# Performance work log

Measured on AMD Instinct MI355X. Metric: run time of the kernel, lower is better.

Reference implementation:

```python
import jax, jax.numpy as jnp
import numpy as np
import math

B_, H_, W_ = 2, 32, 32
DM, DS = 192, 16
RK = math.ceil(DM / 16)  # dt_rank 'auto'
DI = 2 * DM              # d_inner = expand_factor * d_model


def setup_inputs() -> dict:
    key = jax.random.key(0)
    ks = jax.random.split(key, 8)
    x = jax.random.normal(ks[0], (B_, H_, W_, DM), jnp.float32)
    W_in = jax.random.normal(ks[1], (DM, DI), jnp.float32) * 0.02
    b_in = jnp.zeros((DI,), jnp.float32)
    W_x = jax.random.normal(ks[2], (DI, 2 * RK + 2 * DS), jnp.float32) * 0.02
    b_x = jnp.zeros((2 * RK + 2 * DS,), jnp.float32)
    std = RK ** -0.5
    W_dtT = jax.random.uniform(ks[3], (RK, DI), jnp.float32, -std, std)
    W_dtL = jax.random.uniform(ks[4], (RK, DI), jnp.float32, -std, std)
    # dt bias init exactly as in the torch module
    dt = jnp.exp(jax.random.uniform(ks[5], (DI,), jnp.float32)
                 * (math.log(0.1) - math.log(0.001)) + math.log(0.001))
    dt = jnp.clip(dt, 1e-4)
    inv_dt = dt + jnp.log(-jnp.expm1(-dt))
    A = jnp.tile(jnp.arange(1, DS + 1, dtype=jnp.float32), (DI, 1))
    AT_log = jnp.log(A)
    AL_log = jnp.log(A)
    D = jnp.ones((DI,), jnp.float32)
    W_out = jax.random.normal(ks[6], (DI, DM), jnp.float32) * 0.02
    b_out = jnp.zeros((DM,), jnp.float32)
    return dict(x=x, W_in=W_in, b_in=b_in, W_x=W_x, b_x=b_x,
                W_dtT=W_dtT, b_dtT=inv_dt, W_dtL=W_dtL, b_dtL=inv_dt,
                AT_log=AT_log, AL_log=AL_log, D=D, W_out=W_out, b_out=b_out)


def _wavefront_scan(dAT, dAL, bx):
    """2D wavefront linear recurrence over an (H, W) grid.
    h[i,j] = 0.5*dAT[i,j]*h[i-1,j] + 0.5*dAL[i,j]*h[i,j-1] + bx[i,j]
    Inputs: (B, H, W, d_inner, d_state). Sequential over rows (lax.scan),
    parallel linear recurrence along columns (associative_scan)."""
    def combine(c1, c2):
        a1, u1 = c1
        a2, u2 = c2
        return a2 * a1, a2 * u1 + u2

    def row_step(h_prev, row):
        dAT_r, dAL_r, bx_r = row                     # (B, W, di, ds)
        u = 0.5 * dAT_r * h_prev + bx_r              # top contribution folded in
        a = 0.5 * dAL_r
        _, h = jax.lax.associative_scan(combine, (a, u), axis=1)
        return h, h

    rows = (jnp.moveaxis(dAT, 1, 0), jnp.moveaxis(dAL, 1, 0), jnp.moveaxis(bx, 1, 0))
    h0 = jnp.zeros(dAT.shape[:1] + dAT.shape[2:], dAT.dtype)
    _, hs = jax.lax.scan(row_step, h0, rows)         # (H, B, W, di, ds)
    return jnp.moveaxis(hs, 0, 1)                    # (B, H, W, di, ds)


def reference(x, W_in, b_in, W_x, b_x, W_dtT, b_dtT, W_dtL, b_dtL,
              AT_log, AL_log, D, W_out, b_out):
    # in_proj + GELU (torch nn.GELU default = exact erf)
    h = jax.nn.gelu(x @ W_in + b_in, approximate=False)   # (B,H,W,DI)
    # proj_and_discretise
    dbc = h @ W_x + b_x
    dT, dL, Bm, Cm = jnp.split(dbc, [RK, 2 * RK, 2 * RK + DS], axis=-1)
    deltaT = jax.nn.softplus(dT @ W_dtT + b_dtT)          # (B,H,W,DI)
    deltaL = jax.nn.softplus(dL @ W_dtL + b_dtL)
    AT = -jnp.exp(AT_log)                                  # (DI,DS)
    AL = -jnp.exp(AL_log)
    dAT = jnp.exp(deltaT[..., None] * AT)                  # (B,H,W,DI,DS)
    dAL = jnp.exp(deltaL[..., None] * AL)
    BXT = (deltaT * h)[..., None] * Bm[..., None, :]       # delta*B*x
    BXL = (deltaL * h)[..., None] * Bm[..., None, :]
    # 2D wavefront selective scan
    hs = _wavefront_scan(dAT, dAL, 0.5 * (BXT + BXL))
    y = jnp.einsum('bhwds,bhws->bhwd', hs, Cm) + h * D
    # act2 + out_proj
    y = jax.nn.gelu(y, approximate=False)
    return y @ W_out + b_out
```

## Files before the change

### kernel.cpp

```cpp
#include <hip/hip_runtime.h>
#include <math.h>

#define TOK 2048
#define DMOD 192
#define DI 384
#define DS 16
#define RK 12
#define NCOL 56
#define HH 32
#define WW 32
#define BB 2
#define TA 8
#define HSP 388

__device__ __forceinline__ float gelu_exact(float x) {
    return 0.5f * x * (1.0f + erff(x * 0.70710678118654752f));
}
__device__ __forceinline__ float softplus_f(float x) {
    return (x > 20.0f) ? x : log1pf(expf(x));
}
__device__ __forceinline__ float bperm(int byte_addr, float v) {
    return __uint_as_float((unsigned)__builtin_amdgcn_ds_bpermute(
        byte_addr, (int)__float_as_uint(v)));
}

__global__ void k0_transWx(const float* __restrict__ W_x, float* __restrict__ W_xT) {
    int c = blockIdx.x, k = threadIdx.x;
    W_xT[c * DI + k] = W_x[k * NCOL + c];
}

__global__ __launch_bounds__(DI) void K_A(
        const float* __restrict__ x, const float* __restrict__ W_in,
        const float* __restrict__ b_in, const float* __restrict__ W_xT,
        const float* __restrict__ b_x, const float* __restrict__ W_dtT,
        const float* __restrict__ b_dtT, const float* __restrict__ W_dtL,
        const float* __restrict__ b_dtL,
        float* __restrict__ ht, float* __restrict__ dTt, float* __restrict__ dLt,
        float* __restrict__ Bs, float* __restrict__ Cs) {
    __shared__ float xs[TA * DMOD];
    __shared__ float hs[TA * HSP];
    __shared__ float dbcS[TA][NCOL];
    int tid = threadIdx.x;
    int tok0 = blockIdx.x * TA;

    const float* xg = x + (long)tok0 * DMOD;
#pragma unroll
    for (int q = 0; q < 4; ++q) xs[q * DI + tid] = xg[q * DI + tid];
    __syncthreads();

    float acc[TA];
    float bi = b_in[tid];
#pragma unroll
    for (int t = 0; t < TA; ++t) acc[t] = bi;
    for (int k = 0; k < DMOD; k += 4) {
        float w0 = W_in[(k + 0) * DI + tid];
        float w1 = W_in[(k + 1) * DI + tid];
        float w2 = W_in[(k + 2) * DI + tid];
        float w3 = W_in[(k + 3) * DI + tid];
#pragma unroll
        for (int t = 0; t < TA; ++t) {
            float4 xv = *(const float4*)&xs[t * DMOD + k];
            acc[t] = fmaf(xv.x, w0, acc[t]);
            acc[t] = fmaf(xv.y, w1, acc[t]);
            acc[t] = fmaf(xv.z, w2, acc[t]);
            acc[t] = fmaf(xv.w, w3, acc[t]);
        }
    }
#pragma unroll
    for (int t = 0; t < TA; ++t) hs[t * HSP + tid] = gelu_exact(acc[t]);
    __syncthreads();

    for (int oi = tid; oi < TA * NCOL; oi += DI) {
        int tk = oi / NCOL, c = oi - tk * NCOL;
        float p = b_x[c];
        const float* hrow = &hs[tk * HSP];
        const float4* wr = (const float4*)(W_xT + c * DI);
        for (int k = 0; k < DI; k += 4) {
            float4 hv = *(const float4*)&hrow[k];
            float4 wv = wr[k >> 2];
            p = fmaf(hv.x, wv.x, p);  p = fmaf(hv.y, wv.y, p);
            p = fmaf(hv.z, wv.z, p);  p = fmaf(hv.w, wv.w, p);
        }
        dbcS[tk][c] = p;
    }
    __syncthreads();

    int d = tid;
    float aT[TA], aL[TA];
    float bT = b_dtT[d], bL = b_dtL[d];
#pragma unroll
    for (int t = 0; t < TA; ++t) { aT[t] = bT; aL[t] = bL; }
#pragma unroll
    for (int r = 0; r < RK; ++r) {
        float wT = W_dtT[r * DI + d];
        float wL = W_dtL[r * DI + d];
#pragma unroll
        for (int t = 0; t < TA; ++t) {
            aT[t] = fmaf(dbcS[t][r],      wT, aT[t]);
            aL[t] = fmaf(dbcS[t][RK + r], wL, aL[t]);
        }
    }
    int b = tok0 >> 10;
    long ob = (long)(b * DI + d) * 1024 + (tok0 & 1023);
    float v[TA];
#pragma unroll
    for (int t = 0; t < TA; ++t) v[t] = softplus_f(aT[t]);
    *(float4*)&dTt[ob]     = make_float4(v[0], v[1], v[2], v[3]);
    *(float4*)&dTt[ob + 4] = make_float4(v[4], v[5], v[6], v[7]);
#pragma unroll
    for (int t = 0; t < TA; ++t) v[t] = softplus_f(aL[t]);
    *(float4*)&dLt[ob]     = make_float4(v[0], v[1], v[2], v[3]);
    *(float4*)&dLt[ob + 4] = make_float4(v[4], v[5], v[6], v[7]);
#pragma unroll
    for (int t = 0; t < TA; ++t) v[t] = hs[t * HSP + d];
    *(float4*)&ht[ob]     = make_float4(v[0], v[1], v[2], v[3]);
    *(float4*)&ht[ob + 4] = make_float4(v[4], v[5], v[6], v[7]);
    if (tid < 128) {
        int s = tid >> 3, tt = tid & 7;
        long o = (long)(b * DS + s) * 1024 + (tok0 & 1023) + tt;
        Bs[o] = dbcS[tt][2 * RK + s];
        Cs[o] = dbcS[tt][2 * RK + DS + s];
    }
}

__global__ __launch_bounds__(256) void k3_scan(
        const float* __restrict__ dTt, const float* __restrict__ dLt,
        const float* __restrict__ ht, const float* __restrict__ Bs,
        const float* __restrict__ Cs, const float* __restrict__ AT_log,
        const float* __restrict__ AL_log, const float* __restrict__ Dv,
        float* __restrict__ yt) {
    __shared__ float part[8][HH][WW];
    int bd = blockIdx.x;
    int b = bd / DI, d = bd - b * DI;
    int tid = threadIdx.x;
    int w = tid >> 6, lane = tid & 63;
    int s1 = lane >> 5, j = lane & 31;
    int p = w * 2 + s1;

    float AT0 = -__expf(AT_log[d * DS + 2 * p]);
    float AT1 = -__expf(AT_log[d * DS + 2 * p + 1]);
    float AL0 = -__expf(AL_log[d * DS + 2 * p]);
    float AL1 = -__expf(AL_log[d * DS + 2 * p + 1]);

    const float* dTr = dTt + (long)bd * 1024;
    const float* dLr = dLt + (long)bd * 1024;
    const float* hr  = ht  + (long)bd * 1024;
    const float* B0r = Bs + (long)(b * DS + 2 * p) * 1024;
    const float* B1r = B0r + 1024;
    const float* C0r = Cs + (long)(b * DS + 2 * p) * 1024;
    const float* C1r = C0r + 1024;

    int ba1  = ((j >= 1  ? lane - 1  : lane) << 2);
    int ba2  = ((j >= 2  ? lane - 2  : lane) << 2);
    int ba4  = ((j >= 4  ? lane - 4  : lane) << 2);
    int ba8  = ((j >= 8  ? lane - 8  : lane) << 2);
    int ba16 = ((j >= 16 ? lane - 16 : lane) << 2);

    float hp0 = 0.f, hp1 = 0.f;
    float nT = dTr[j], nL = dLr[j], nh = hr[j];
    float nB0 = B0r[j], nB1 = B1r[j], nC0 = C0r[j], nC1 = C1r[j];

#pragma unroll 1
    for (int i = 0; i < HH; ++i) {
        float cT = nT, cL = nL, chv = nh;
        float cB0 = nB0, cB1 = nB1, cC0 = nC0, cC1 = nC1;
        int nx = (i + 1 < HH) ? (i + 1) * 32 + j : j;
        nT = dTr[nx]; nL = dLr[nx]; nh = hr[nx];
        nB0 = B0r[nx]; nB1 = B1r[nx]; nC0 = C0r[nx]; nC1 = C1r[nx];

        float g  = 0.5f * (cT + cL) * chv;
        float a0 = 0.5f * __expf(cL * AL0);
        float a1 = 0.5f * __expf(cL * AL1);
        float u0 = fmaf(0.5f * __expf(cT * AT0), hp0, g * cB0);
        float u1 = fmaf(0.5f * __expf(cT * AT1), hp1, g * cB1);

#define SCAN_STEP(BA, OFF)                                            \
        {                                                             \
            float au0 = bperm(BA, a0), uu0 = bperm(BA, u0);           \
            float au1 = bperm(BA, a1), uu1 = bperm(BA, u1);           \
            bool m = (j >= OFF);                                      \
            uu0 = m ? uu0 : 0.f;  au0 = m ? au0 : 1.f;                \
            uu1 = m ? uu1 : 0.f;  au1 = m ? au1 : 1.f;                \
            u0 = fmaf(a0, uu0, u0);  a0 *= au0;                       \
            u1 = fmaf(a1, uu1, u1);  a1 *= au1;                       \
        }
        SCAN_STEP(ba1, 1)  SCAN_STEP(ba2, 2)  SCAN_STEP(ba4, 4)
        SCAN_STEP(ba8, 8)  SCAN_STEP(ba16, 16)
#undef SCAN_STEP

        hp0 = u0;  hp1 = u1;
        part[p][i][j] = fmaf(u0, cC0, u1 * cC1);
    }
    __syncthreads();

    float Dd = Dv[d];
    float* yr = yt + (long)bd * 1024;
#pragma unroll
    for (int q = 0; q < 4; ++q) {
        int cell = q * 256 + tid;
        float sum = part[0][0][cell] + part[1][0][cell] + part[2][0][cell] +
                    part[3][0][cell] + part[4][0][cell] + part[5][0][cell] +
                    part[6][0][cell] + part[7][0][cell];
        yr[cell] = gelu_exact(sum + hr[cell] * Dd);
    }
}

__global__ __launch_bounds__(DMOD) void K_out(
        const float* __restrict__ yt, const float* __restrict__ W_out,
        const float* __restrict__ b_out, float* __restrict__ out) {
    int n = threadIdx.x;
    int tok0 = blockIdx.x * TA;
    int b = tok0 >> 10;
    const float* yb = yt + (long)b * DI * 1024 + (tok0 & 1023);
    float acc[TA];
    float bo = b_out[n];
#pragma unroll
    for (int t = 0; t < TA; ++t) acc[t] = bo;
    for (int dd = 0; dd < DI; ++dd) {
        float w = W_out[dd * DMOD + n];
        const float* yp = yb + (long)dd * 1024;
        float4 y0 = *(const float4*)yp;
        float4 y1 = *(const float4*)(yp + 4);
        acc[0] = fmaf(y0.x, w, acc[0]);  acc[1] = fmaf(y0.y, w, acc[1]);
        acc[2] = fmaf(y0.z, w, acc[2]);  acc[3] = fmaf(y0.w, w, acc[3]);
        acc[4] = fmaf(y1.x, w, acc[4]);  acc[5] = fmaf(y1.y, w, acc[5]);
        acc[6] = fmaf(y1.z, w, acc[6]);  acc[7] = fmaf(y1.w, w, acc[7]);
    }
#pragma unroll
    for (int t = 0; t < TA; ++t)
        out[(long)(tok0 + t) * DMOD + n] = acc[t];
}

extern "C" void kernel_launch(void* const* d_in, const int* in_sizes, int n_in,
                              void* d_out, int out_size, void* d_ws, size_t ws_size,
                              hipStream_t stream) {
    const float* x      = (const float*)d_in[0];
    const float* W_in   = (const float*)d_in[1];
    const float* b_in   = (const float*)d_in[2];
    const float* W_x    = (const float*)d_in[3];
    const float* b_x    = (const float*)d_in[4];
    const float* W_dtT  = (const float*)d_in[5];
    const float* b_dtT  = (const float*)d_in[6];
    const float* W_dtL  = (const float*)d_in[7];
    const float* b_dtL  = (const float*)d_in[8];
    const float* AT_log = (const float*)d_in[9];
    const float* AL_log = (const float*)d_in[10];
    const float* Dv     = (const float*)d_in[11];
    const float* W_out  = (const float*)d_in[12];
    const float* b_out  = (const float*)d_in[13];
    float* out = (float*)d_out;

    float* ws = (float*)d_ws;
    const long NE = (long)BB * DI * 1024;
    float* ht   = ws;
    float* dTt  = ws + NE;
    float* dLt  = ws + 2 * NE;
    float* Bs   = ws + 3 * NE;
    float* Cs   = Bs + (long)BB * DS * 1024;
    float* W_xT = Cs + (long)BB * DS * 1024;
    float* yt   = dTt;

    k0_transWx<<<NCOL, DI, 0, stream>>>(W_x, W_xT);
    K_A<<<TOK / TA, DI, 0, stream>>>(x, W_in, b_in, W_xT, b_x,
                                     W_dtT, b_dtT, W_dtL, b_dtL,
                                     ht, dTt, dLt, Bs, Cs);
    k3_scan<<<BB * DI, 256, 0, stream>>>(dTt, dLt, ht, Bs, Cs,
                                         AT_log, AL_log, Dv, yt);
    K_out<<<TOK / TA, DMOD, 0, stream>>>(yt, W_out, b_out, out);
}
```

Before: 177.8 us.

## Split projection kernel and compute delta softplus inside scan kernel

Replaces the monolithic K_A kernel with a separate in_proj+GELU kernel (more blocks, 128 threads) and a dedicated x_proj kernel that writes all 56 dbc columns channel-major. The dt projection and softplus move into the scan kernel, which computes deltaT/deltaL for its channel into shared memory, so the full-size dT/dL tensors no longer make a round trip through global memory. The W_x transpose kernel is dropped and the output projection tile shrinks to 4 tokens for more parallelism. In exchange, every scan block recomputes the 24-term dt projection from global dbc, and there are smaller tiles with less weight reuse.

```diff
diff --git a/kernel.cpp b/kernel.cpp
--- a/kernel.cpp
+++ b/kernel.cpp
@@ -10,8 +10,6 @@
 #define HH 32
 #define WW 32
 #define BB 2
-#define TA 8
-#define HSP 388
 
 __device__ __forceinline__ float gelu_exact(float x) {
     return 0.5f * x * (1.0f + erff(x * 0.70710678118654752f));
@@ -24,41 +22,30 @@
         byte_addr, (int)__float_as_uint(v)));
 }
 
-__global__ void k0_transWx(const float* __restrict__ W_x, float* __restrict__ W_xT) {
-    int c = blockIdx.x, k = threadIdx.x;
-    W_xT[c * DI + k] = W_x[k * NCOL + c];
-}
-
-__global__ __launch_bounds__(DI) void K_A(
+__global__ __launch_bounds__(128) void K_h(
         const float* __restrict__ x, const float* __restrict__ W_in,
-        const float* __restrict__ b_in, const float* __restrict__ W_xT,
-        const float* __restrict__ b_x, const float* __restrict__ W_dtT,
-        const float* __restrict__ b_dtT, const float* __restrict__ W_dtL,
-        const float* __restrict__ b_dtL,
-        float* __restrict__ ht, float* __restrict__ dTt, float* __restrict__ dLt,
-        float* __restrict__ Bs, float* __restrict__ Cs) {
-    __shared__ float xs[TA * DMOD];
-    __shared__ float hs[TA * HSP];
-    __shared__ float dbcS[TA][NCOL];
-    int tid = threadIdx.x;
-    int tok0 = blockIdx.x * TA;
-
+        const float* __restrict__ b_in, float* __restrict__ h_tm,
+        float* __restrict__ ht) {
+    __shared__ float xs[4 * DMOD];
+    int tx = threadIdx.x;
+    int n = blockIdx.x * 128 + tx;
+    int tok0 = blockIdx.y * 4;
     const float* xg = x + (long)tok0 * DMOD;
 #pragma unroll
-    for (int q = 0; q < 4; ++q) xs[q * DI + tid] = xg[q * DI + tid];
+    for (int q = 0; q < 6; ++q) xs[q * 128 + tx] = xg[q * 128 + tx];
     __syncthreads();
-
-    float acc[TA];
-    float bi = b_in[tid];
-#pragma unroll
-    for (int t = 0; t < TA; ++t) acc[t] = bi;
+    float acc[4];
+    float bi = b_in[n];
+#pragma unroll
+    for (int t = 0; t < 4; ++t) acc[t] = bi;
+#pragma unroll 2
     for (int k = 0; k < DMOD; k += 4) {
-        float w0 = W_in[(k + 0) * DI + tid];
-        float w1 = W_in[(k + 1) * DI + tid];
-        float w2 = W_in[(k + 2) * DI + tid];
-        float w3 = W_in[(k + 3) * DI + tid];
-#pragma unroll
-        for (int t = 0; t < TA; ++t) {
+        float w0 = W_in[(k + 0) * DI + n];
+        float w1 = W_in[(k + 1) * DI + n];
+        float w2 = W_in[(k + 2) * DI + n];
+        float w3 = W_in[(k + 3) * DI + n];
+#pragma unroll
+        for (int t = 0; t < 4; ++t) {
             float4 xv = *(const float4*)&xs[t * DMOD + k];
             acc[t] = fmaf(xv.x, w0, acc[t]);
             acc[t] = fmaf(xv.y, w1, acc[t]);
@@ -66,73 +53,83 @@
             acc[t] = fmaf(xv.w, w3, acc[t]);
         }
     }
-#pragma unroll
-    for (int t = 0; t < TA; ++t) hs[t * HSP + tid] = gelu_exact(acc[t]);
-    __syncthreads();
-
-    for (int oi = tid; oi < TA * NCOL; oi += DI) {
-        int tk = oi / NCOL, c = oi - tk * NCOL;
-        float p = b_x[c];
-        const float* hrow = &hs[tk * HSP];
-        const float4* wr = (const float4*)(W_xT + c * DI);
-        for (int k = 0; k < DI; k += 4) {
-            float4 hv = *(const float4*)&hrow[k];
-            float4 wv = wr[k >> 2];
-            p = fmaf(hv.x, wv.x, p);  p = fmaf(hv.y, wv.y, p);
-            p = fmaf(hv.z, wv.z, p);  p = fmaf(hv.w, wv.w, p);
-        }
-        dbcS[tk][c] = p;
-    }
-    __syncthreads();
-
-    int d = tid;
-    float aT[TA], aL[TA];
-    float bT = b_dtT[d], bL = b_dtL[d];
-#pragma unroll
-    for (int t = 0; t < TA; ++t) { aT[t] = bT; aL[t] = bL; }
-#pragma unroll
-    for (int r = 0; r < RK; ++r) {
-        float wT = W_dtT[r * DI + d];
-        float wL = W_dtL[r * DI + d];
-#pragma unroll
-        for (int t = 0; t < TA; ++t) {
-            aT[t] = fmaf(dbcS[t][r],      wT, aT[t]);
-            aL[t] = fmaf(dbcS[t][RK + r], wL, aL[t]);
-        }
-    }
-    int b = tok0 >> 10;
-    long ob = (long)(b * DI + d) * 1024 + (tok0 & 1023);
-    float v[TA];
-#pragma unroll
-    for (int t = 0; t < TA; ++t) v[t] = softplus_f(aT[t]);
-    *(float4*)&dTt[ob]     = make_float4(v[0], v[1], v[2], v[3]);
-    *(float4*)&dTt[ob + 4] = make_float4(v[4], v[5], v[6], v[7]);
-#pragma unroll
-    for (int t = 0; t < TA; ++t) v[t] = softplus_f(aL[t]);
-    *(float4*)&dLt[ob]     = make_float4(v[0], v[1], v[2], v[3]);
-    *(float4*)&dLt[ob + 4] = make_float4(v[4], v[5], v[6], v[7]);
-#pragma unroll
-    for (int t = 0; t < TA; ++t) v[t] = hs[t * HSP + d];
-    *(float4*)&ht[ob]     = make_float4(v[0], v[1], v[2], v[3]);
-    *(float4*)&ht[ob + 4] = make_float4(v[4], v[5], v[6], v[7]);
-    if (tid < 128) {
-        int s = tid >> 3, tt = tid & 7;
-        long o = (long)(b * DS + s) * 1024 + (tok0 & 1023) + tt;
-        Bs[o] = dbcS[tt][2 * RK + s];
-        Cs[o] = dbcS[tt][2 * RK + DS + s];
+    float hv[4];
+#pragma unroll
+    for (int t = 0; t < 4; ++t) {
+        hv[t] = gelu_exact(acc[t]);
+        h_tm[(long)(tok0 + t) * DI + n] = hv[t];
+    }
+    int b = tok0 >> 10, ij = tok0 & 1023;
+    *(float4*)&ht[(long)(b * DI + n) * 1024 + ij] =
+        make_float4(hv[0], hv[1], hv[2], hv[3]);
+}
+
+__global__ __launch_bounds__(128) void K_dbc(
+        const float* __restrict__ h_tm, const float* __restrict__ W_x,
+        const float* __restrict__ b_x, float* __restrict__ dbcT) {
+    int tid = threadIdx.x;
+    int c = tid & 63;
+    int ce = (c < NCOL) ? c : 0;
+    int mA = __builtin_amdgcn_readfirstlane(blockIdx.x * 4 + (tid >> 6) * 2);
+    const float* hA = h_tm + (long)mA * DI;
+    const float* hB = hA + DI;
+    const float* Wp = W_x + ce;
+    float a0 = 0.f, a1 = 0.f, b0 = 0.f, b1 = 0.f;
+#pragma unroll 2
+    for (int k = 0; k < DI; k += 4) {
+        float w0 = Wp[(k + 0) * NCOL], w1 = Wp[(k + 1) * NCOL];
+        float w2 = Wp[(k + 2) * NCOL], w3 = Wp[(k + 3) * NCOL];
+        a0 = fmaf(hA[k + 0], w0, a0);  a1 = fmaf(hA[k + 1], w1, a1);
+        a0 = fmaf(hA[k + 2], w2, a0);  a1 = fmaf(hA[k + 3], w3, a1);
+        b0 = fmaf(hB[k + 0], w0, b0);  b1 = fmaf(hB[k + 1], w1, b1);
+        b0 = fmaf(hB[k + 2], w2, b0);  b1 = fmaf(hB[k + 3], w3, b1);
+    }
+    if (c < NCOL) {
+        float bx = b_x[c];
+        int b = mA >> 10, ij = mA & 1023;
+        long o = (long)(b * NCOL + c) * 1024 + ij;
+        dbcT[o]     = a0 + a1 + bx;
+        dbcT[o + 1] = b0 + b1 + bx;
     }
 }
 
 __global__ __launch_bounds__(256) void k3_scan(
-        const float* __restrict__ dTt, const float* __restrict__ dLt,
-        const float* __restrict__ ht, const float* __restrict__ Bs,
-        const float* __restrict__ Cs, const float* __restrict__ AT_log,
-        const float* __restrict__ AL_log, const float* __restrict__ Dv,
-        float* __restrict__ yt) {
+        const float* __restrict__ ht, const float* __restrict__ dbcT,
+        const float* __restrict__ W_dtT, const float* __restrict__ b_dtT,
+        const float* __restrict__ W_dtL, const float* __restrict__ b_dtL,
+        const float* __restrict__ AT_log, const float* __restrict__ AL_log,
+        const float* __restrict__ Dv, float* __restrict__ yt) {
     __shared__ float part[8][HH][WW];
+    __shared__ float ldT[1024];
+    __shared__ float ldL[1024];
     int bd = blockIdx.x;
     int b = bd / DI, d = bd - b * DI;
     int tid = threadIdx.x;
+    const float* db = dbcT + (long)b * NCOL * 1024;
+
+    {
+        float wTr[RK], wLr[RK];
+#pragma unroll
+        for (int r = 0; r < RK; ++r) {
+            wTr[r] = W_dtT[r * DI + d];
+            wLr[r] = W_dtL[r * DI + d];
+        }
+        float bT = b_dtT[d], bL = b_dtL[d];
+#pragma unroll
+        for (int q = 0; q < 4; ++q) {
+            int cell = q * 256 + tid;
+            float aT = bT, aL = bL;
+#pragma unroll
+            for (int r = 0; r < RK; ++r) {
+                aT = fmaf(db[(long)r * 1024 + cell],        wTr[r], aT);
+                aL = fmaf(db[(long)(RK + r) * 1024 + cell], wLr[r], aL);
+            }
+            ldT[cell] = softplus_f(aT);
+            ldL[cell] = softplus_f(aL);
+        }
+    }
+    __syncthreads();
+
     int w = tid >> 6, lane = tid & 63;
     int s1 = lane >> 5, j = lane & 31;
     int p = w * 2 + s1;
@@ -142,12 +139,10 @@
     float AL0 = -__expf(AL_log[d * DS + 2 * p]);
     float AL1 = -__expf(AL_log[d * DS + 2 * p + 1]);
 
-    const float* dTr = dTt + (long)bd * 1024;
-    const float* dLr = dLt + (long)bd * 1024;
-    const float* hr  = ht  + (long)bd * 1024;
-    const float* B0r = Bs + (long)(b * DS + 2 * p) * 1024;
+    const float* hr  = ht + (long)bd * 1024;
+    const float* B0r = db + (long)(24 + 2 * p) * 1024;
     const float* B1r = B0r + 1024;
-    const float* C0r = Cs + (long)(b * DS + 2 * p) * 1024;
+    const float* C0r = db + (long)(40 + 2 * p) * 1024;
     const float* C1r = C0r + 1024;
 
     int ba1  = ((j >= 1  ? lane - 1  : lane) << 2);
@@ -157,17 +152,19 @@
     int ba16 = ((j >= 16 ? lane - 16 : lane) << 2);
 
     float hp0 = 0.f, hp1 = 0.f;
-    float nT = dTr[j], nL = dLr[j], nh = hr[j];
+    float nh = hr[j];
     float nB0 = B0r[j], nB1 = B1r[j], nC0 = C0r[j], nC1 = C1r[j];
 
 #pragma unroll 1
     for (int i = 0; i < HH; ++i) {
-        float cT = nT, cL = nL, chv = nh;
+        float chv = nh;
         float cB0 = nB0, cB1 = nB1, cC0 = nC0, cC1 = nC1;
         int nx = (i + 1 < HH) ? (i + 1) * 32 + j : j;
-        nT = dTr[nx]; nL = dLr[nx]; nh = hr[nx];
+        nh = hr[nx];
         nB0 = B0r[nx]; nB1 = B1r[nx]; nC0 = C0r[nx]; nC1 = C1r[nx];
 
+        float cT = ldT[i * 32 + j];
+        float cL = ldL[i * 32 + j];
         float g  = 0.5f * (cT + cL) * chv;
         float a0 = 0.5f * __expf(cL * AL0);
         float a1 = 0.5f * __expf(cL * AL1);
@@ -195,12 +192,14 @@
 
     float Dd = Dv[d];
     float* yr = yt + (long)bd * 1024;
+    const float* pf = &part[0][0][0];
 #pragma unroll
     for (int q = 0; q < 4; ++q) {
         int cell = q * 256 + tid;
-        float sum = part[0][0][cell] + part[1][0][cell] + part[2][0][cell] +
-                    part[3][0][cell] + part[4][0][cell] + part[5][0][cell] +
-                    part[6][0][cell] + part[7][0][cell];
+        float sum = pf[cell]           + pf[1024 + cell] +
+                    pf[2 * 1024 + cell] + pf[3 * 1024 + cell] +
+                    pf[4 * 1024 + cell] + pf[5 * 1024 + cell] +
+                    pf[6 * 1024 + cell] + pf[7 * 1024 + cell];
         yr[cell] = gelu_exact(sum + hr[cell] * Dd);
     }
 }
@@ -209,25 +208,24 @@
         const float* __restrict__ yt, const float* __restrict__ W_out,
         const float* __restrict__ b_out, float* __restrict__ out) {
     int n = threadIdx.x;
-    int tok0 = blockIdx.x * TA;
+    int tok0 = blockIdx.x * 4;
     int b = tok0 >> 10;
     const float* yb = yt + (long)b * DI * 1024 + (tok0 & 1023);
-    float acc[TA];
+    float acc[4];
     float bo = b_out[n];
 #pragma unroll
-    for (int t = 0; t < TA; ++t) acc[t] = bo;
+    for (int t = 0; t < 4; ++t) acc[t] = bo;
+#pragma unroll 2
     for (int dd = 0; dd < DI; ++dd) {
         float w = W_out[dd * DMOD + n];
-        const float* yp = yb + (long)dd * 1024;
-        float4 y0 = *(const float4*)yp;
-        float4 y1 = *(const float4*)(yp + 4);
-        acc[0] = fmaf(y0.x, w, acc[0]);  acc[1] = fmaf(y0.y, w, acc[1]);
-        acc[2] = fmaf(y0.z, w, acc[2]);  acc[3] = fmaf(y0.w, w, acc[3]);
-        acc[4] = fmaf(y1.x, w, acc[4]);  acc[5] = fmaf(y1.y, w, acc[5]);
-        acc[6] = fmaf(y1.z, w, acc[6]);  acc[7] = fmaf(y1.w, w, acc[7]);
-    }
-#pragma unroll
-    for (int t = 0; t < TA; ++t)
+        float4 y4 = *(const float4*)(yb + (long)dd * 1024);
+        acc[0] = fmaf(y4.x, w, acc[0]);
+        acc[1] = fmaf(y4.y, w, acc[1]);
+        acc[2] = fmaf(y4.z, w, acc[2]);
+        acc[3] = fmaf(y4.w, w, acc[3]);
+    }
+#pragma unroll
+    for (int t = 0; t < 4; ++t)
         out[(long)(tok0 + t) * DMOD + n] = acc[t];
 }
 
@@ -252,19 +250,15 @@
 
     float* ws = (float*)d_ws;
     const long NE = (long)BB * DI * 1024;
-    float* ht   = ws;
-    float* dTt  = ws + NE;
-    float* dLt  = ws + 2 * NE;
-    float* Bs   = ws + 3 * NE;
-    float* Cs   = Bs + (long)BB * DS * 1024;
-    float* W_xT = Cs + (long)BB * DS * 1024;
-    float* yt   = dTt;
-
-    k0_transWx<<<NCOL, DI, 0, stream>>>(W_x, W_xT);
-    K_A<<<TOK / TA, DI, 0, stream>>>(x, W_in, b_in, W_xT, b_x,
-                                     W_dtT, b_dtT, W_dtL, b_dtL,
-                                     ht, dTt, dLt, Bs, Cs);
-    k3_scan<<<BB * DI, 256, 0, stream>>>(dTt, dLt, ht, Bs, Cs,
+    float* h_tm = ws;
+    float* ht   = ws + NE;
+    float* dbcT = ws + 2 * NE;
+    float* yt   = ht;
+
+    K_h  <<<dim3(3, TOK / 4), 128, 0, stream>>>(x, W_in, b_in, h_tm, ht);
+    K_dbc<<<TOK / 4, 128, 0, stream>>>(h_tm, W_x, b_x, dbcT);
+    k3_scan<<<BB * DI, 256, 0, stream>>>(ht, dbcT,
+                                         W_dtT, b_dtT, W_dtL, b_dtL,
                                          AT_log, AL_log, Dv, yt);
-    K_out<<<TOK / TA, DMOD, 0, stream>>>(yt, W_out, b_out, out);
-}
+    K_out<<<TOK / 4, DMOD, 0, stream>>>(yt, W_out, b_out, out);
+}
```

After: 197.5 us. 11.1% more time.
